# Kernel tuning notes

Hardware: AMD Instinct MI355X
Metric: run time of the kernel (lower is better)

The kernel has to match this reference:

```python
import jax, jax.numpy as jnp
import numpy as np

B, D_IN, UNITS = 2048, 4096, 4096

def setup_inputs() -> dict:
    key = jax.random.key(0)
    k_x, k_m, k_w, k_b = jax.random.split(key, 4)
    x = jax.random.normal(k_x, (B, D_IN), dtype=jnp.float32)
    mask = jax.random.randint(k_m, (D_IN, UNITS), 0, 2).astype(jnp.float32)
    # glorot_uniform kernel
    limit = np.sqrt(6.0 / (D_IN + UNITS)).astype(np.float32)
    W = jax.random.uniform(k_w, (D_IN, UNITS), dtype=jnp.float32, minval=-limit, maxval=limit)
    b = jnp.zeros((UNITS,), dtype=jnp.float32)
    return {"x": x, "mask": mask, "W": W, "b": b}

def reference(x, mask, W, b):
    # Original: build COO sparse tensor of kernel entries where mask != 0,
    # then (sparse_W^T @ x^T)^T == x @ (W masked by mask != 0). Bias added, no activation.
    W_masked = jnp.where(mask != 0.0, W, jnp.zeros((), dtype=W.dtype))
    return x @ W_masked + b
```

## Files before the change

kernel.cpp:

```cpp
#include <hip/hip_runtime.h>

#define M_DIM 2048
#define K_DIM 4096
#define N_DIM 4096

typedef unsigned short u16;
typedef unsigned int u32;
typedef __bf16 bf16x8 __attribute__((ext_vector_type(8)));
typedef float f32x4 __attribute__((ext_vector_type(4)));
typedef float f4 __attribute__((ext_vector_type(4)));
typedef u16 u16x8 __attribute__((ext_vector_type(8)));
typedef u32 u32x4 __attribute__((ext_vector_type(4)));

__device__ __forceinline__ u16 f2bf(float f) {
    unsigned int u = __float_as_uint(f);
    u += 0x7fffu + ((u >> 16) & 1u);
    return (u16)(u >> 16);
}

__device__ __forceinline__ u32 pack2(float lo, float hi) {
    u32 a = __float_as_uint(lo); a += 0x7fffu + ((a >> 16) & 1u);
    u32 b = __float_as_uint(hi); b += 0x7fffu + ((b >> 16) & 1u);
    return (a >> 16) | (b & 0xffff0000u);
}

__device__ __forceinline__ void load16(const void* g, void* l) {
    __builtin_amdgcn_global_load_lds(
        (__attribute__((address_space(1))) const void*)g,
        (__attribute__((address_space(3))) void*)l,
        16, 0, 0);
}

__global__ __launch_bounds__(256) void prep(const float* __restrict__ x,
                                            u16* __restrict__ xb,
                                            const float* __restrict__ W,
                                            const float* __restrict__ Msk,
                                            u16* __restrict__ Bt) {
    const int t = threadIdx.x;
    if (blockIdx.x >= 2048) {
        size_t i = ((size_t)(blockIdx.x - 2048) * 256 + t) * 16;
#pragma unroll
        for (int h = 0; h < 2; ++h) {
            f4 v0 = *(const f4*)(x + i + h * 8);
            f4 v1 = *(const f4*)(x + i + h * 8 + 4);
            u16x8 o;
            o[0] = f2bf(v0[0]); o[1] = f2bf(v0[1]); o[2] = f2bf(v0[2]); o[3] = f2bf(v0[3]);
            o[4] = f2bf(v1[0]); o[5] = f2bf(v1[1]); o[6] = f2bf(v1[2]); o[7] = f2bf(v1[3]);
            *(u16x8*)(xb + i + h * 8) = o;
        }
        return;
    }
    const int n0 = (blockIdx.x & 31) * 128;
    const int k0 = (blockIdx.x >> 5) * 64;
    const int ko = t & 7;
    const int ng = t >> 3;

    const float* Wp = W   + (size_t)(k0 + 8 * ko) * N_DIM + n0 + 4 * ng;
    const float* Mp = Msk + (size_t)(k0 + 8 * ko) * N_DIM + n0 + 4 * ng;

    f4 a[8];
#pragma unroll
    for (int j = 0; j < 8; ++j) {
        f4 wv = *(const f4*)(Wp + (size_t)j * N_DIM);
        f4 mv = *(const f4*)(Mp + (size_t)j * N_DIM);
        a[j][0] = mv[0] != 0.f ? wv[0] : 0.f;
        a[j][1] = mv[1] != 0.f ? wv[1] : 0.f;
        a[j][2] = mv[2] != 0.f ? wv[2] : 0.f;
        a[j][3] = mv[3] != 0.f ? wv[3] : 0.f;
    }

    u16* bp = Bt + (size_t)(n0 + 4 * ng) * K_DIM + k0 + 8 * ko;
#pragma unroll
    for (int i = 0; i < 4; ++i) {
        u32x4 o;
        o[0] = pack2(a[0][i], a[1][i]);
        o[1] = pack2(a[2][i], a[3][i]);
        o[2] = pack2(a[4][i], a[5][i]);
        o[3] = pack2(a[6][i], a[7][i]);
        *(u32x4*)(bp + (size_t)i * K_DIM) = o;
    }
}

__global__ __launch_bounds__(256) void gemm_bt(const u16* __restrict__ A,
                                               const u16* __restrict__ Bt,
                                               const float* __restrict__ bias,
                                               float* __restrict__ C) {
    __shared__ __align__(16) u16 As[128 * 64];
    __shared__ __align__(16) u16 Bs[128 * 64];

    const int t  = threadIdx.x;
    const int bn = blockIdx.x;
    const int bm = blockIdx.y;

    const int srow   = t >> 3;
    const int schunk = (t & 7) ^ (srow & 7);
    const u16* gA = A  + (size_t)(bm * 128 + srow) * K_DIM + schunk * 8;
    const u16* gB = Bt + (size_t)(bn * 128 + srow) * K_DIM + schunk * 8;
    u16* lA = As + t * 8;
    u16* lB = Bs + t * 8;

    const int lane = t & 63;
    const int wave = t >> 6;
    const int wm = (wave >> 1) * 64;
    const int wn = (wave & 1) * 64;
    const int fr = lane & 15;
    const int q  = lane >> 4;
    const int sw = fr & 7;
    const int col0 = ((0 + q) ^ sw) * 8;
    const int col1 = ((4 + q) ^ sw) * 8;

    f32x4 acc[4][4] = {};

    for (int k0 = 0; k0 < K_DIM; k0 += 64) {
#pragma unroll
        for (int it = 0; it < 4; ++it) {
            load16(gA + k0 + it * 32 * K_DIM, lA + it * 2048);
            load16(gB + k0 + it * 32 * K_DIM, lB + it * 2048);
        }
        __syncthreads();
#pragma unroll
        for (int kx = 0; kx < 2; ++kx) {
            const int col = kx ? col1 : col0;
            bf16x8 af[4], bfr[4];
#pragma unroll
            for (int i = 0; i < 4; ++i)
                af[i] = *(const bf16x8*)(As + (wm + i * 16 + fr) * 64 + col);
#pragma unroll
            for (int j = 0; j < 4; ++j)
                bfr[j] = *(const bf16x8*)(Bs + (wn + j * 16 + fr) * 64 + col);
#pragma unroll
            for (int i = 0; i < 4; ++i)
#pragma unroll
                for (int j = 0; j < 4; ++j)
                    acc[i][j] = __builtin_amdgcn_mfma_f32_16x16x32_bf16(
                        af[i], bfr[j], acc[i][j], 0, 0, 0);
        }
        __syncthreads();
    }

    const int rb = q * 4;
#pragma unroll
    for (int i = 0; i < 4; ++i) {
#pragma unroll
        for (int j = 0; j < 4; ++j) {
            int n = bn * 128 + wn + j * 16 + fr;
            float bv = bias[n];
#pragma unroll
            for (int r = 0; r < 4; ++r) {
                int m = bm * 128 + wm + i * 16 + rb + r;
                C[(size_t)m * N_DIM + n] = acc[i][j][r] + bv;
            }
        }
    }
}

extern "C" void kernel_launch(void* const* d_in, const int* in_sizes, int n_in,
                              void* d_out, int out_size, void* d_ws, size_t ws_size,
                              hipStream_t stream) {
    const float* x    = (const float*)d_in[0];
    const float* mask = (const float*)d_in[1];
    const float* W    = (const float*)d_in[2];
    const float* bias = (const float*)d_in[3];
    float* out = (float*)d_out;

    u16* Bt = (u16*)d_ws;
    u16* xb = (u16*)d_ws + (size_t)N_DIM * K_DIM;

    prep<<<4096, 256, 0, stream>>>(x, xb, W, mask, Bt);
    gemm_bt<<<dim3(N_DIM / 128, M_DIM / 128), 256, 0, stream>>>(xb, Bt, bias, out);
}
```

Measured before the change: 251.8 us.

## Use 8-wave 128x256 GEMM tiles with double-buffered LDS and interleaved prefetch

Replaces the 4-wave 128x128 GEMM with a 512-thread kernel computing 128x256 tiles. LDS is double-buffered, and global-to-LDS loads for the next K tile are split into three chunks interleaved with quarter-tile MFMA groups. Synchronisation uses explicit vmcnt waits and barriers, and MFMA bursts get raised priority via s_setprio. The goal is to hide load latency behind compute and improve operand reuse, at the cost of more LDS per block and fragile hand-tuned waitcnt accounting.

```diff
diff --git a/kernel.cpp b/kernel.cpp
--- a/kernel.cpp
+++ b/kernel.cpp
@@ -3,6 +3,7 @@
 #define M_DIM 2048
 #define K_DIM 4096
 #define N_DIM 4096
+#define KTILES (K_DIM / 64)
 
 typedef unsigned short u16;
 typedef unsigned int u32;
@@ -81,12 +82,12 @@
     }
 }
 
-__global__ __launch_bounds__(256) void gemm_bt(const u16* __restrict__ A,
-                                               const u16* __restrict__ Bt,
-                                               const float* __restrict__ bias,
-                                               float* __restrict__ C) {
-    __shared__ __align__(16) u16 As[128 * 64];
-    __shared__ __align__(16) u16 Bs[128 * 64];
+__global__ __launch_bounds__(512, 2) void gemm8(const u16* __restrict__ A,
+                                                const u16* __restrict__ Bt,
+                                                const float* __restrict__ bias,
+                                                float* __restrict__ C) {
+    __shared__ __align__(16) u16 As[2][128 * 64];
+    __shared__ __align__(16) u16 Bs[2][256 * 64];
 
     const int t  = threadIdx.x;
     const int bn = blockIdx.x;
@@ -95,47 +96,78 @@
     const int srow   = t >> 3;
     const int schunk = (t & 7) ^ (srow & 7);
     const u16* gA = A  + (size_t)(bm * 128 + srow) * K_DIM + schunk * 8;
-    const u16* gB = Bt + (size_t)(bn * 128 + srow) * K_DIM + schunk * 8;
-    u16* lA = As + t * 8;
-    u16* lB = Bs + t * 8;
+    const u16* gB = Bt + (size_t)(bn * 256 + srow) * K_DIM + schunk * 8;
 
     const int lane = t & 63;
-    const int wave = t >> 6;
-    const int wm = (wave >> 1) * 64;
-    const int wn = (wave & 1) * 64;
+    const int wv   = t >> 6;
+    const int wm = (wv >> 2) * 64;
+    const int wn = (wv & 3) * 64;
     const int fr = lane & 15;
     const int q  = lane >> 4;
     const int sw = fr & 7;
     const int col0 = ((0 + q) ^ sw) * 8;
     const int col1 = ((4 + q) ^ sw) * 8;
 
+#define STAGE_A(buf, kt) do { \
+    load16(gA + (size_t)(kt) * 64,               (buf) + t * 8); \
+    load16(gA + (size_t)(kt) * 64 + 64 * K_DIM,  (buf) + 4096 + t * 8); } while (0)
+#define STAGE_B0(buf, kt) do { \
+    load16(gB + (size_t)(kt) * 64,               (buf) + t * 8); \
+    load16(gB + (size_t)(kt) * 64 + 64 * K_DIM,  (buf) + 4096 + t * 8); } while (0)
+#define STAGE_B1(buf, kt) do { \
+    load16(gB + (size_t)(kt) * 64 + 128 * K_DIM, (buf) + 8192 + t * 8); \
+    load16(gB + (size_t)(kt) * 64 + 192 * K_DIM, (buf) + 12288 + t * 8); } while (0)
+
+#define RD(dst, base, row0) do { \
+    dst[0][0] = *(const bf16x8*)((base) + ((row0) + fr) * 64 + col0); \
+    dst[0][1] = *(const bf16x8*)((base) + ((row0) + fr) * 64 + col1); \
+    dst[1][0] = *(const bf16x8*)((base) + ((row0) + 16 + fr) * 64 + col0); \
+    dst[1][1] = *(const bf16x8*)((base) + ((row0) + 16 + fr) * 64 + col1); } while (0)
+
+#define MM(fa, fb, mq, nq) do { \
+    __builtin_amdgcn_s_setprio(1); \
+    _Pragma("unroll") \
+    for (int kx = 0; kx < 2; ++kx) \
+      _Pragma("unroll") \
+      for (int i2 = 0; i2 < 2; ++i2) \
+        _Pragma("unroll") \
+        for (int j2 = 0; j2 < 2; ++j2) \
+          acc[(mq) * 2 + i2][(nq) * 2 + j2] = __builtin_amdgcn_mfma_f32_16x16x32_bf16( \
+              fa[i2][kx], fb[j2][kx], acc[(mq) * 2 + i2][(nq) * 2 + j2], 0, 0, 0); \
+    __builtin_amdgcn_s_setprio(0); } while (0)
+
     f32x4 acc[4][4] = {};
 
-    for (int k0 = 0; k0 < K_DIM; k0 += 64) {
-#pragma unroll
-        for (int it = 0; it < 4; ++it) {
-            load16(gA + k0 + it * 32 * K_DIM, lA + it * 2048);
-            load16(gB + k0 + it * 32 * K_DIM, lB + it * 2048);
-        }
-        __syncthreads();
-#pragma unroll
-        for (int kx = 0; kx < 2; ++kx) {
-            const int col = kx ? col1 : col0;
-            bf16x8 af[4], bfr[4];
-#pragma unroll
-            for (int i = 0; i < 4; ++i)
-                af[i] = *(const bf16x8*)(As + (wm + i * 16 + fr) * 64 + col);
-#pragma unroll
-            for (int j = 0; j < 4; ++j)
-                bfr[j] = *(const bf16x8*)(Bs + (wn + j * 16 + fr) * 64 + col);
-#pragma unroll
-            for (int i = 0; i < 4; ++i)
-#pragma unroll
-                for (int j = 0; j < 4; ++j)
-                    acc[i][j] = __builtin_amdgcn_mfma_f32_16x16x32_bf16(
-                        af[i], bfr[j], acc[i][j], 0, 0, 0);
-        }
-        __syncthreads();
+    STAGE_A(As[0], 0);
+    STAGE_B0(Bs[0], 0);
+    STAGE_B1(Bs[0], 0);
+
+    for (int kt = 0; kt < KTILES; ++kt) {
+        const int cur = kt & 1;
+        const int nxt = cur ^ 1;
+        const int kn  = (kt + 1) & (KTILES - 1);
+        const u16* a = As[cur];
+        const u16* b = Bs[cur];
+        bf16x8 fA0[2][2], fA1[2][2], fB0[2][2], fB1[2][2];
+
+        asm volatile("s_waitcnt vmcnt(2) lgkmcnt(0)" ::: "memory");
+        __builtin_amdgcn_s_barrier();
+        RD(fA0, a, wm);
+        RD(fB0, b, wn);
+        STAGE_A(As[nxt], kn);
+        MM(fA0, fB0, 0, 0);
+
+        asm volatile("s_waitcnt vmcnt(2) lgkmcnt(0)" ::: "memory");
+        __builtin_amdgcn_s_barrier();
+        RD(fB1, b, wn + 32);
+        STAGE_B0(Bs[nxt], kn);
+        MM(fA0, fB1, 0, 1);
+
+        RD(fA1, a, wm + 32);
+        STAGE_B1(Bs[nxt], kn);
+        MM(fA1, fB1, 1, 1);
+
+        MM(fA1, fB0, 1, 0);
     }
 
     const int rb = q * 4;
@@ -143,7 +175,7 @@
     for (int i = 0; i < 4; ++i) {
 #pragma unroll
         for (int j = 0; j < 4; ++j) {
-            int n = bn * 128 + wn + j * 16 + fr;
+            int n = bn * 256 + wn + j * 16 + fr;
             float bv = bias[n];
 #pragma unroll
             for (int r = 0; r < 4; ++r) {
@@ -152,6 +184,11 @@
             }
         }
     }
+#undef STAGE_A
+#undef STAGE_B0
+#undef STAGE_B1
+#undef RD
+#undef MM
 }
 
 extern "C" void kernel_launch(void* const* d_in, const int* in_sizes, int n_in,
@@ -167,5 +204,5 @@
     u16* xb = (u16*)d_ws + (size_t)N_DIM * K_DIM;
 
     prep<<<4096, 256, 0, stream>>>(x, xb, W, mask, Bt);
-    gemm_bt<<<dim3(N_DIM / 128, M_DIM / 128), 256, 0, stream>>>(xb, Bt, bias, out);
-}
+    gemm8<<<dim3(N_DIM / 256, M_DIM / 128), 512, 0, stream>>>(xb, Bt, bias, out);
+}
```

Result: slower. 265.4 us (+5.4%).
